# Kernel tuning notes

Measured on AMD Instinct MI355X. Metric: run time of the kernel, lower is better.

Reference implementation:

```python
import jax, jax.numpy as jnp
import numpy as np

N = 50000      # nodes
E = 800000     # directed edges (avg degree 16 in/out pairs)
F_IN = 16      # dataset.num_features
H = 64         # neuron
S = 7          # Chebyshev order


def setup_inputs() -> dict:
    key = jax.random.key(0)
    ks = jax.random.split(key, 12)
    x = jax.random.normal(ks[0], (N, F_IN), dtype=jnp.float32)
    row = jax.random.randint(ks[1], (E,), 0, N, dtype=jnp.int32)
    off = jax.random.randint(ks[2], (E,), 1, N, dtype=jnp.int32)
    col = (row + off) % N  # guarantees no self-loops (PyG removes them)
    edge_index = jnp.stack([row, col])
    lambda_max = jnp.array([2.0], dtype=jnp.float32)
    def lin(k, fi, fo):
        return jax.random.normal(k, (S, fi, fo), dtype=jnp.float32) * (1.0 / np.sqrt(fi))
    W1 = lin(ks[3], F_IN, H); b1 = jnp.zeros((H,), jnp.float32)
    W2 = lin(ks[4], H, H);    b2 = jnp.zeros((H,), jnp.float32)
    W3 = lin(ks[5], H, H);    b3 = jnp.zeros((H,), jnp.float32)
    Wfc = jax.random.normal(ks[6], (H, 1), dtype=jnp.float32) * (1.0 / np.sqrt(H))
    bfc = jnp.zeros((1,), jnp.float32)
    return {"x": x, "edge_index": edge_index, "lambda_max": lambda_max,
            "W1": W1, "b1": b1, "W2": W2, "b2": b2, "W3": W3, "b3": b3,
            "Wfc": Wfc, "bfc": bfc}


def _make_spmv(edge_index, lam, n):
    # L_hat = 2/lambda_max * (I - D^-1/2 A D^-1/2) - I  (PyG ChebConv sym norm)
    row, col = edge_index[0], edge_index[1]
    deg = jax.ops.segment_sum(jnp.ones_like(row, dtype=jnp.float32), row, num_segments=n)
    dis = jnp.where(deg > 0, jax.lax.rsqrt(jnp.maximum(deg, 1.0)), 0.0)
    w = -(2.0 / lam) * dis[row] * dis[col]      # off-diagonal edge weights
    diag = 2.0 / lam - 1.0                       # self-loop weight
    def spmv(xx):  # L_hat @ xx
        return jax.ops.segment_sum(w[:, None] * xx[col], row, num_segments=n) + diag * xx
    return spmv


def _cheb(xx, W, b, spmv):
    Tx0 = xx
    out = Tx0 @ W[0]
    Tx1 = spmv(Tx0)
    out = out + Tx1 @ W[1]
    for k in range(2, W.shape[0]):  # fixed small S loop
        Tx2 = 2.0 * spmv(Tx1) - Tx0
        out = out + Tx2 @ W[k]
        Tx0, Tx1 = Tx1, Tx2
    return out + b


def reference(x, edge_index, lambda_max, W1, b1, W2, b2, W3, b3, Wfc, bfc):
    lam = lambda_max[0]
    spmv = _make_spmv(edge_index, lam, x.shape[0])
    h = jax.nn.relu(_cheb(x, W1, b1, spmv))
    h = jax.nn.relu(_cheb(h, W2, b2, spmv))
    h = jax.nn.relu(_cheb(h, W3, b3, spmv))
    return h @ Wfc + bfc
```

## Files before the change

kernel.cpp:

```cpp
#include <hip/hip_runtime.h>
#include <math.h>


#define WS_ALIGN(x) (((size_t)(x) + 255) & ~(size_t)255)

using f16x8 = __attribute__((ext_vector_type(8))) _Float16;
using f32x4 = __attribute__((ext_vector_type(4))) float;

__device__ inline float h2f_bits(unsigned int b) {
  unsigned short s = (unsigned short)(b & 0xffffu);
  _Float16 h;
  __builtin_memcpy(&h, &s, 2);
  return (float)h;
}
__device__ inline unsigned short f2h_bits(float f) {
  _Float16 h = (_Float16)f;
  unsigned short s;
  __builtin_memcpy(&s, &h, 2);
  return s;
}
union H4 {
  ushort4 u;
  _Float16 h[4];
};

__global__ __launch_bounds__(256) void hist_kernel(const int* __restrict__ row, int E,
                                                   int* __restrict__ deg) {
  int i = blockIdx.x * 256 + threadIdx.x;
  if (i < E) atomicAdd(&deg[row[i]], 1);
}

__global__ __launch_bounds__(256) void scan_sum_kernel(const int* __restrict__ deg,
                                                       int* __restrict__ bsum, int n) {
  int base = blockIdx.x * 1024 + threadIdx.x;
  int v = 0;
#pragma unroll
  for (int u = 0; u < 4; ++u) {
    int i = base + u * 256;
    if (i < n) v += deg[i];
  }
#pragma unroll
  for (int off = 32; off > 0; off >>= 1) v += __shfl_down(v, off, 64);
  __shared__ int ws[4];
  int lane = threadIdx.x & 63, wave = threadIdx.x >> 6;
  if (lane == 0) ws[wave] = v;
  __syncthreads();
  if (threadIdx.x == 0) bsum[blockIdx.x] = ws[0] + ws[1] + ws[2] + ws[3];
}

__global__ __launch_bounds__(64) void scan_bsum_kernel(int* __restrict__ bsum, int nb) {
  int t = threadIdx.x;
  int v = (t < nb) ? bsum[t] : 0;
  int sc = v;
#pragma unroll
  for (int off = 1; off < 64; off <<= 1) {
    int tv = __shfl_up(sc, off, 64);
    if (t >= off) sc += tv;
  }
  if (t < nb) bsum[t] = sc - v;
}

__global__ __launch_bounds__(256) void scan_out_kernel(const int* __restrict__ deg,
                                                       const int* __restrict__ bsum,
                                                       int* __restrict__ row_ptr,
                                                       int* __restrict__ cursor,
                                                       float* __restrict__ dis, int n) {
  int base = blockIdx.x * 1024 + threadIdx.x * 4;
  int loc[4];
  int s = 0;
#pragma unroll
  for (int u = 0; u < 4; ++u) {
    int i = base + u;
    loc[u] = (i < n) ? deg[i] : 0;
    s += loc[u];
  }
  int lane = threadIdx.x & 63, wave = threadIdx.x >> 6;
  int sc = s;
#pragma unroll
  for (int off = 1; off < 64; off <<= 1) {
    int tv = __shfl_up(sc, off, 64);
    if (lane >= off) sc += tv;
  }
  __shared__ int wtot[4];
  if (lane == 63) wtot[wave] = sc;
  __syncthreads();
  int pre = sc - s + bsum[blockIdx.x];
  for (int w = 0; w < wave; ++w) pre += wtot[w];
  if (blockIdx.x == 0 && threadIdx.x == 0) row_ptr[0] = 0;
  int running = pre;
#pragma unroll
  for (int u = 0; u < 4; ++u) {
    int i = base + u;
    if (i < n) {
      cursor[i] = running;
      dis[i] = (loc[u] > 0) ? (1.0f / sqrtf((float)loc[u])) : 0.0f;
      running += loc[u];
      row_ptr[i + 1] = running;
    }
  }
}

__global__ __launch_bounds__(256) void scatter_kernel(const int* __restrict__ row,
                                                      const int* __restrict__ col, int E,
                                                      int* __restrict__ cursor,
                                                      const float* __restrict__ dis,
                                                      const float* __restrict__ lamp,
                                                      unsigned int* __restrict__ cw) {
  int i = blockIdx.x * 256 + threadIdx.x;
  if (i >= E) return;
  int r = row[i], c = col[i];
  int pos = atomicAdd(&cursor[r], 1);
  float w = -(2.0f / lamp[0]) * dis[r] * dis[c];
  cw[pos] = ((unsigned int)c << 16) | (unsigned int)f2h_bits(w);
}

__global__ __launch_bounds__(256) void x_to_slots_kernel(const float* __restrict__ x,
                                                         ushort* __restrict__ T1, int n) {
  int t = blockIdx.x * 256 + threadIdx.x;
  if (t < n * 4) {
    int row = t >> 2, q = t & 3;
    float4 v = ((const float4*)x)[(size_t)row * 4 + q];
    ushort4 o;
    o.x = f2h_bits(v.x);
    o.y = f2h_bits(v.y);
    o.z = f2h_bits(v.z);
    o.w = f2h_bits(v.w);
    ((ushort4*)T1)[(size_t)row * 4 + q] = o;
  } else if (t < n * 8) {
    int t2 = t - n * 4;
    ((ushort4*)(T1 + (size_t)7 * n * 16))[t2] = make_ushort4(0, 0, 0, 0);
  }
}

template <int KREAL, int KT>
__global__ __launch_bounds__(256) void wpk_prep(const float* __restrict__ W,
                                                ushort* __restrict__ Wpk) {
  int t = blockIdx.x * 256 + threadIdx.x;
  if (t >= KT * 256) return;
  int kt = t >> 8, nt = (t >> 6) & 3, l = t & 63;
  int col = nt * 16 + (l & 15);
  int kb = kt * 32 + ((l >> 4) << 3);
  ushort tmp[8];
#pragma unroll
  for (int j = 0; j < 8; ++j) {
    int k = kb + j;
    float v = (k < KREAL) ? W[(size_t)k * 64 + col] : 0.0f;
    tmp[j] = f2h_bits(v);
  }
  ushort4* dst = (ushort4*)Wpk + (size_t)((kt * 4 + nt) * 64 + l) * 2;
  dst[0] = make_ushort4(tmp[0], tmp[1], tmp[2], tmp[3]);
  dst[1] = make_ushort4(tmp[4], tmp[5], tmp[6], tmp[7]);
}

template <int SW, int MODE, int SLICES>
__global__ __launch_bounds__(256) void spmv_slice(const int* __restrict__ row_ptr,
                                                  const unsigned int* __restrict__ cw,
                                                  const float* __restrict__ lamp,
                                                  const ushort4* __restrict__ xin,
                                                  const ushort4* __restrict__ sub,
                                                  ushort4* __restrict__ xout, int ssz4,
                                                  int n) {
  constexpr int LPR = SW / 4;
  constexpr int RPB = 256 / LPR;
  constexpr int EPL = 16 / LPR;
  int bx = blockIdx.x;
  if (SLICES == 2) {
    int sl = bx & 1;
    bx >>= 1;
    xin += (size_t)sl * ssz4;
    if (MODE == 1) sub += (size_t)sl * ssz4;
    xout += (size_t)sl * ssz4;
  }
  int i = bx * RPB + threadIdx.y;
  if (i >= n) return;
  int f4 = threadIdx.x;
  int lane = (threadIdx.y * LPR + f4) & 63;
  int grpbase = lane - f4;
  float diag = 2.0f / lamp[0] - 1.0f;
  H4 xd;
  xd.u = xin[(size_t)i * LPR + f4];
  float4 a = make_float4(diag * (float)xd.h[0], diag * (float)xd.h[1],
                         diag * (float)xd.h[2], diag * (float)xd.h[3]);
  int s = row_ptr[i], e = row_ptr[i + 1];

  for (int j0 = s; j0 < e; j0 += 16) {
    unsigned int pv[EPL];
#pragma unroll
    for (int u = 0; u < EPL; ++u) {
      int jj = j0 + f4 * EPL + u;
      pv[u] = cw[jj < e ? jj : (e - 1)];
    }
    H4 xv[16];
    float ww[16];
#pragma unroll
    for (int u = 0; u < 16; ++u) {
      unsigned int pu = (unsigned int)__shfl((int)pv[u % EPL], grpbase + u / EPL, 64);
      bool valid = (j0 + u) < e;
      ww[u] = valid ? h2f_bits(pu) : 0.0f;
      int ad = valid ? (int)(pu >> 16) : i;
      xv[u].u = xin[(size_t)ad * LPR + f4];
    }
#pragma unroll
    for (int u = 0; u < 16; ++u) {
      a.x += ww[u] * (float)xv[u].h[0];
      a.y += ww[u] * (float)xv[u].h[1];
      a.z += ww[u] * (float)xv[u].h[2];
      a.w += ww[u] * (float)xv[u].h[3];
    }
  }

  float4 r;
  if (MODE == 1) {
    H4 sv;
    sv.u = sub[(size_t)i * LPR + f4];
    r = make_float4(2.0f * a.x - (float)sv.h[0], 2.0f * a.y - (float)sv.h[1],
                    2.0f * a.z - (float)sv.h[2], 2.0f * a.w - (float)sv.h[3]);
  } else {
    r = a;
  }
  H4 o;
  o.u.x = f2h_bits(r.x);
  o.u.y = f2h_bits(r.y);
  o.u.z = f2h_bits(r.z);
  o.u.w = f2h_bits(r.w);
  xout[(size_t)i * LPR + f4] = o.u;
}

template <int SW, int KT, bool LAST>
__global__ __launch_bounds__(256) void gemm_mfma(const ushort* __restrict__ A,
                                                 const ushort* __restrict__ Wpk,
                                                 const float* __restrict__ bias,
                                                 ushort* __restrict__ dsth,
                                                 float* __restrict__ dacc, int n) {
  int l = threadIdx.x & 63;
  int tile = blockIdx.x * 4 + (threadIdx.x >> 6);
  int r0 = tile * 16;
  if (r0 >= n) return;
  size_t slotsz = (size_t)n * SW;
  int row = r0 + (l & 15);
  const f16x8* bp = (const f16x8*)Wpk + l;
  f32x4 c[4] = {{0.f, 0.f, 0.f, 0.f},
                {0.f, 0.f, 0.f, 0.f},
                {0.f, 0.f, 0.f, 0.f},
                {0.f, 0.f, 0.f, 0.f}};
#pragma unroll
  for (int kt = 0; kt < KT; ++kt) {
    int slot, off;
    if constexpr (SW == 32) {
      slot = kt;
      off = (l >> 4) << 3;
    } else {
      slot = 2 * kt + ((l >> 4) >> 1);
      off = ((l >> 4) & 1) << 3;
    }
    f16x8 af = *(const f16x8*)(A + slot * slotsz + (size_t)row * SW + off);
#pragma unroll
    for (int nt = 0; nt < 4; ++nt) {
      f16x8 bf = bp[(kt * 4 + nt) * 64];
      c[nt] = __builtin_amdgcn_mfma_f32_16x16x32_f16(af, bf, c[nt], 0, 0, 0);
    }
  }
  int rb = r0 + ((l >> 4) << 2);
  int cc = l & 15;
  size_t dslot = (size_t)n * 32;
#pragma unroll
  for (int nt = 0; nt < 4; ++nt) {
    int col = nt * 16 + cc;
    if (LAST) {
#pragma unroll
      for (int j = 0; j < 4; ++j) dacc[(size_t)(rb + j) * 64 + col] = c[nt][j];
    } else {
      float bv = bias[col];
      ushort* dbase = dsth + (col >> 5) * dslot + (col & 31);
#pragma unroll
      for (int j = 0; j < 4; ++j) {
        float v = fmaxf(c[nt][j] + bv, 0.0f);
        dbase[(size_t)(rb + j) * 32] = f2h_bits(v);
      }
    }
  }
}

__global__ __launch_bounds__(256) void fc_fused_kernel(const float* __restrict__ acc,
                                                       const float* __restrict__ b,
                                                       const float* __restrict__ Wfc,
                                                       const float* __restrict__ bfc,
                                                       float* __restrict__ out, int n) {
  int i = blockIdx.x * 4 + threadIdx.y;
  if (i >= n) return;
  int l = threadIdx.x;
  float v = fmaxf(acc[(size_t)i * 64 + l] + b[l], 0.0f) * Wfc[l];
#pragma unroll
  for (int off = 32; off > 0; off >>= 1) v += __shfl_down(v, off, 64);
  if (l == 0) out[i] = v + bfc[0];
}

extern "C" void kernel_launch(void* const* d_in, const int* in_sizes, int n_in, void* d_out,
                              int out_size, void* d_ws, size_t ws_size, hipStream_t stream) {
  const float* x = (const float*)d_in[0];
  const int* ei = (const int*)d_in[1];
  const float* lamp = (const float*)d_in[2];
  const float* W1 = (const float*)d_in[3];
  const float* b1 = (const float*)d_in[4];
  const float* W2 = (const float*)d_in[5];
  const float* b2 = (const float*)d_in[6];
  const float* W3 = (const float*)d_in[7];
  const float* b3 = (const float*)d_in[8];
  const float* Wfc = (const float*)d_in[9];
  const float* bfc = (const float*)d_in[10];

  const int N = in_sizes[0] / 16;
  const int E = in_sizes[1] / 2;
  const int* row = ei;
  const int* col = ei + E;

  char* p = (char*)d_ws;
  auto alloc = [&](size_t bytes) {
    char* r = p;
    p += WS_ALIGN(bytes);
    return r;
  };
  int* deg = (int*)alloc((size_t)N * 4);
  int* row_ptr = (int*)alloc((size_t)(N + 1) * 4);
  int* cursor = (int*)alloc((size_t)N * 4);
  unsigned int* cw = (unsigned int*)alloc((size_t)E * 4);
  float* dis = (float*)alloc((size_t)N * 4);
  int* bsum = (int*)alloc(256 * 4);
  ushort* T1 = (ushort*)alloc((size_t)8 * N * 16 * 2);
  ushort* TXC = (ushort*)alloc((size_t)14 * N * 32 * 2);
  float* acc = (float*)alloc((size_t)N * 64 * 4);
  ushort* Wpk1 = (ushort*)alloc((size_t)4 * 256 * 8 * 2);
  ushort* Wpk2 = (ushort*)alloc((size_t)14 * 256 * 8 * 2);
  ushort* Wpk3 = (ushort*)alloc((size_t)14 * 256 * 8 * 2);
  (void)ws_size;
  (void)n_in;
  (void)out_size;

  (void)hipMemsetAsync(deg, 0, (size_t)N * 4, stream);
  hist_kernel<<<(E + 255) / 256, 256, 0, stream>>>(row, E, deg);
  int nb = (N + 1023) / 1024;
  scan_sum_kernel<<<nb, 256, 0, stream>>>(deg, bsum, N);
  scan_bsum_kernel<<<1, 64, 0, stream>>>(bsum, nb);
  scan_out_kernel<<<nb, 256, 0, stream>>>(deg, bsum, row_ptr, cursor, dis, N);
  scatter_kernel<<<(E + 255) / 256, 256, 0, stream>>>(row, col, E, cursor, dis, lamp, cw);

  x_to_slots_kernel<<<(N * 8 + 255) / 256, 256, 0, stream>>>(x, T1, N);
  wpk_prep<112, 4><<<4, 256, 0, stream>>>(W1, Wpk1);
  wpk_prep<448, 14><<<14, 256, 0, stream>>>(W2, Wpk2);
  wpk_prep<448, 14><<<14, 256, 0, stream>>>(W3, Wpk3);

  {
    int ssz4 = N * 4;
    auto S = [&](int k) { return (ushort4*)T1 + (size_t)k * ssz4; };
    dim3 bs(4, 64);
    int gs = (N + 63) / 64;
    spmv_slice<16, 0, 1><<<gs, bs, 0, stream>>>(row_ptr, cw, lamp, S(0), nullptr, S(1), ssz4,
                                                N);
    for (int k = 2; k < 7; ++k)
      spmv_slice<16, 1, 1><<<gs, bs, 0, stream>>>(row_ptr, cw, lamp, S(k - 1), S(k - 2), S(k),
                                                  ssz4, N);
    gemm_mfma<16, 4, false><<<(N / 16 + 3) / 4 + 1, 256, 0, stream>>>(T1, Wpk1, b1, TXC,
                                                                      nullptr, N);
  }

  for (int layer = 2; layer <= 3; ++layer) {
    int ssz4 = N * 8;
    auto S = [&](int k) { return (ushort4*)TXC + (size_t)(2 * k) * ssz4; };
    dim3 bs(8, 32);
    int gs = 2 * ((N + 31) / 32);
    spmv_slice<32, 0, 2><<<gs, bs, 0, stream>>>(row_ptr, cw, lamp, S(0), nullptr, S(1), ssz4,
                                                N);
    for (int k = 2; k < 7; ++k)
      spmv_slice<32, 1, 2><<<gs, bs, 0, stream>>>(row_ptr, cw, lamp, S(k - 1), S(k - 2), S(k),
                                                  ssz4, N);
    if (layer == 2)
      gemm_mfma<32, 14, false><<<(N / 16 + 3) / 4 + 1, 256, 0, stream>>>(TXC, Wpk2, b2, TXC,
                                                                         nullptr, N);
    else
      gemm_mfma<32, 14, true><<<(N / 16 + 3) / 4 + 1, 256, 0, stream>>>(TXC, Wpk3, nullptr,
                                                                        nullptr, acc, N);
  }

  fc_fused_kernel<<<(N + 3) / 4, dim3(64, 4), 0, stream>>>(acc, b3, Wfc, bfc, (float*)d_out,
                                                           N);
}
```

Measured before the change: 426.1 us.

## Widen SpMV gathers to 16-byte loads and partition CSR scatter by row range

The SpMV kernel now has each lane load 8 fp16 features (16 bytes) per neighbour instead of 4. That halves the lanes per row, doubles the rows per block, and cuts the edge batch from 16 to 8. The CSR scatter kernel becomes a grid-stride kernel where each block group handles only rows in one eighth of the node range, so atomics and writes to cw land in a more localized region. The cost is that every edge is read 8 times in scatter and each SpMV lane carries more register state.

```diff
diff --git a/kernel.cpp b/kernel.cpp
--- a/kernel.cpp
+++ b/kernel.cpp
@@ -19,9 +19,10 @@
   __builtin_memcpy(&s, &h, 2);
   return s;
 }
-union H4 {
-  ushort4 u;
-  _Float16 h[4];
+union H8 {
+  uint4 q;
+  _Float16 h[8];
+  ushort us[8];
 };
 
 __global__ __launch_bounds__(256) void hist_kernel(const int* __restrict__ row, int E,
@@ -100,18 +101,26 @@
   }
 }
 
-__global__ __launch_bounds__(256) void scatter_kernel(const int* __restrict__ row,
-                                                      const int* __restrict__ col, int E,
-                                                      int* __restrict__ cursor,
-                                                      const float* __restrict__ dis,
-                                                      const float* __restrict__ lamp,
-                                                      unsigned int* __restrict__ cw) {
-  int i = blockIdx.x * 256 + threadIdx.x;
-  if (i >= E) return;
-  int r = row[i], c = col[i];
-  int pos = atomicAdd(&cursor[r], 1);
-  float w = -(2.0f / lamp[0]) * dis[r] * dis[c];
-  cw[pos] = ((unsigned int)c << 16) | (unsigned int)f2h_bits(w);
+__global__ __launch_bounds__(256) void scatter_x8(const int* __restrict__ row,
+                                                  const int* __restrict__ col, int E,
+                                                  int* __restrict__ cursor,
+                                                  const float* __restrict__ dis,
+                                                  const float* __restrict__ lamp,
+                                                  unsigned int* __restrict__ cw, int n) {
+  int c = blockIdx.x & 7;
+  int j = blockIdx.x >> 3;
+  int nj = gridDim.x >> 3;
+  int lo = (c * n) >> 3;
+  int hi = ((c + 1) * n) >> 3;
+  float sc = -(2.0f / lamp[0]);
+  for (int i = j * 256 + threadIdx.x; i < E; i += nj * 256) {
+    int r = row[i];
+    if (r < lo || r >= hi) continue;
+    int cc = col[i];
+    int pos = atomicAdd(&cursor[r], 1);
+    float w = sc * dis[r] * dis[cc];
+    cw[pos] = ((unsigned int)cc << 16) | (unsigned int)f2h_bits(w);
+  }
 }
 
 __global__ __launch_bounds__(256) void x_to_slots_kernel(const float* __restrict__ x,
@@ -156,74 +165,72 @@
 __global__ __launch_bounds__(256) void spmv_slice(const int* __restrict__ row_ptr,
                                                   const unsigned int* __restrict__ cw,
                                                   const float* __restrict__ lamp,
-                                                  const ushort4* __restrict__ xin,
-                                                  const ushort4* __restrict__ sub,
-                                                  ushort4* __restrict__ xout, int ssz4,
+                                                  const ushort* __restrict__ xin,
+                                                  const ushort* __restrict__ sub,
+                                                  ushort* __restrict__ xout, int ssz,
                                                   int n) {
-  constexpr int LPR = SW / 4;
+  constexpr int LPR = SW / 8;
   constexpr int RPB = 256 / LPR;
-  constexpr int EPL = 16 / LPR;
+  constexpr int B = 8;
+  constexpr int EPL = B / LPR;
   int bx = blockIdx.x;
   if (SLICES == 2) {
     int sl = bx & 1;
     bx >>= 1;
-    xin += (size_t)sl * ssz4;
-    if (MODE == 1) sub += (size_t)sl * ssz4;
-    xout += (size_t)sl * ssz4;
+    xin += (size_t)sl * ssz;
+    if (MODE == 1) sub += (size_t)sl * ssz;
+    xout += (size_t)sl * ssz;
   }
   int i = bx * RPB + threadIdx.y;
   if (i >= n) return;
-  int f4 = threadIdx.x;
-  int lane = (threadIdx.y * LPR + f4) & 63;
-  int grpbase = lane - f4;
+  int f8 = threadIdx.x;
+  int lane = (threadIdx.y * LPR + f8) & 63;
+  int grpbase = lane - f8;
   float diag = 2.0f / lamp[0] - 1.0f;
-  H4 xd;
-  xd.u = xin[(size_t)i * LPR + f4];
-  float4 a = make_float4(diag * (float)xd.h[0], diag * (float)xd.h[1],
-                         diag * (float)xd.h[2], diag * (float)xd.h[3]);
+  H8 xd;
+  xd.q = *(const uint4*)(xin + (size_t)i * SW + f8 * 8);
+  float a[8];
+#pragma unroll
+  for (int j = 0; j < 8; ++j) a[j] = diag * (float)xd.h[j];
   int s = row_ptr[i], e = row_ptr[i + 1];
 
-  for (int j0 = s; j0 < e; j0 += 16) {
+  for (int j0 = s; j0 < e; j0 += B) {
     unsigned int pv[EPL];
 #pragma unroll
     for (int u = 0; u < EPL; ++u) {
-      int jj = j0 + f4 * EPL + u;
+      int jj = j0 + f8 * EPL + u;
       pv[u] = cw[jj < e ? jj : (e - 1)];
     }
-    H4 xv[16];
-    float ww[16];
-#pragma unroll
-    for (int u = 0; u < 16; ++u) {
+    H8 xv[B];
+    float ww[B];
+#pragma unroll
+    for (int u = 0; u < B; ++u) {
       unsigned int pu = (unsigned int)__shfl((int)pv[u % EPL], grpbase + u / EPL, 64);
       bool valid = (j0 + u) < e;
       ww[u] = valid ? h2f_bits(pu) : 0.0f;
       int ad = valid ? (int)(pu >> 16) : i;
-      xv[u].u = xin[(size_t)ad * LPR + f4];
-    }
-#pragma unroll
-    for (int u = 0; u < 16; ++u) {
-      a.x += ww[u] * (float)xv[u].h[0];
-      a.y += ww[u] * (float)xv[u].h[1];
-      a.z += ww[u] * (float)xv[u].h[2];
-      a.w += ww[u] * (float)xv[u].h[3];
-    }
-  }
-
-  float4 r;
+      xv[u].q = *(const uint4*)(xin + (size_t)ad * SW + f8 * 8);
+    }
+#pragma unroll
+    for (int u = 0; u < B; ++u)
+#pragma unroll
+      for (int j = 0; j < 8; ++j) a[j] += ww[u] * (float)xv[u].h[j];
+  }
+
+  float r[8];
   if (MODE == 1) {
-    H4 sv;
-    sv.u = sub[(size_t)i * LPR + f4];
-    r = make_float4(2.0f * a.x - (float)sv.h[0], 2.0f * a.y - (float)sv.h[1],
-                    2.0f * a.z - (float)sv.h[2], 2.0f * a.w - (float)sv.h[3]);
+    H8 sv;
+    sv.q = *(const uint4*)(sub + (size_t)i * SW + f8 * 8);
+#pragma unroll
+    for (int j = 0; j < 8; ++j) r[j] = 2.0f * a[j] - (float)sv.h[j];
   } else {
-    r = a;
-  }
-  H4 o;
-  o.u.x = f2h_bits(r.x);
-  o.u.y = f2h_bits(r.y);
-  o.u.z = f2h_bits(r.z);
-  o.u.w = f2h_bits(r.w);
-  xout[(size_t)i * LPR + f4] = o.u;
+#pragma unroll
+    for (int j = 0; j < 8; ++j) r[j] = a[j];
+  }
+  H8 o;
+#pragma unroll
+  for (int j = 0; j < 8; ++j) o.us[j] = f2h_bits(r[j]);
+  *(uint4*)(xout + (size_t)i * SW + f8 * 8) = o.q;
 }
 
 template <int SW, int KT, bool LAST>
@@ -342,7 +349,7 @@
   scan_sum_kernel<<<nb, 256, 0, stream>>>(deg, bsum, N);
   scan_bsum_kernel<<<1, 64, 0, stream>>>(bsum, nb);
   scan_out_kernel<<<nb, 256, 0, stream>>>(deg, bsum, row_ptr, cursor, dis, N);
-  scatter_kernel<<<(E + 255) / 256, 256, 0, stream>>>(row, col, E, cursor, dis, lamp, cw);
+  scatter_x8<<<2048, 256, 0, stream>>>(row, col, E, cursor, dis, lamp, cw, N);
 
   x_to_slots_kernel<<<(N * 8 + 255) / 256, 256, 0, stream>>>(x, T1, N);
   wpk_prep<112, 4><<<4, 256, 0, stream>>>(W1, Wpk1);
@@ -350,29 +357,29 @@
   wpk_prep<448, 14><<<14, 256, 0, stream>>>(W3, Wpk3);
 
   {
-    int ssz4 = N * 4;
-    auto S = [&](int k) { return (ushort4*)T1 + (size_t)k * ssz4; };
-    dim3 bs(4, 64);
-    int gs = (N + 63) / 64;
-    spmv_slice<16, 0, 1><<<gs, bs, 0, stream>>>(row_ptr, cw, lamp, S(0), nullptr, S(1), ssz4,
+    int ssz = N * 16;
+    auto S = [&](int k) { return T1 + (size_t)k * ssz; };
+    dim3 bs(2, 128);
+    int gs = (N + 127) / 128;
+    spmv_slice<16, 0, 1><<<gs, bs, 0, stream>>>(row_ptr, cw, lamp, S(0), nullptr, S(1), ssz,
                                                 N);
     for (int k = 2; k < 7; ++k)
       spmv_slice<16, 1, 1><<<gs, bs, 0, stream>>>(row_ptr, cw, lamp, S(k - 1), S(k - 2), S(k),
-                                                  ssz4, N);
+                                                  ssz, N);
     gemm_mfma<16, 4, false><<<(N / 16 + 3) / 4 + 1, 256, 0, stream>>>(T1, Wpk1, b1, TXC,
                                                                       nullptr, N);
   }
 
   for (int layer = 2; layer <= 3; ++layer) {
-    int ssz4 = N * 8;
-    auto S = [&](int k) { return (ushort4*)TXC + (size_t)(2 * k) * ssz4; };
-    dim3 bs(8, 32);
-    int gs = 2 * ((N + 31) / 32);
-    spmv_slice<32, 0, 2><<<gs, bs, 0, stream>>>(row_ptr, cw, lamp, S(0), nullptr, S(1), ssz4,
+    int ssz = N * 32;
+    auto S = [&](int k) { return TXC + (size_t)(2 * k) * ssz; };
+    dim3 bs(4, 64);
+    int gs = 2 * ((N + 63) / 64);
+    spmv_slice<32, 0, 2><<<gs, bs, 0, stream>>>(row_ptr, cw, lamp, S(0), nullptr, S(1), ssz,
                                                 N);
     for (int k = 2; k < 7; ++k)
       spmv_slice<32, 1, 2><<<gs, bs, 0, stream>>>(row_ptr, cw, lamp, S(k - 1), S(k - 2), S(k),
-                                                  ssz4, N);
+                                                  ssz, N);
     if (layer == 2)
       gemm_mfma<32, 14, false><<<(N / 16 + 3) / 4 + 1, 256, 0, stream>>>(TXC, Wpk2, b2, TXC,
                                                                          nullptr, N);
```

After: 400.0 us. 6.1% less time.
